# Optimization experiments

Hardware: AMD Instinct MI355X
Metric: run time of the kernel (lower is better)

Reference implementation:

```python
import jax, jax.numpy as jnp
import numpy as np

N, D = 512, 512
MARGIN = 1.0
NUM_CLASSES = 64


def setup_inputs() -> dict:
    key = jax.random.key(0)
    k1, k2 = jax.random.split(key)
    x = jax.random.normal(k1, (N, D), dtype=jnp.float32)
    x = x / jnp.linalg.norm(x, axis=1, keepdims=True)  # l2-normalized embeddings
    target = jax.random.randint(k2, (N,), 0, NUM_CLASSES)
    return {"input": x, "target": target}


def _pairwise_sq_dist(emb):
    # Faithful to pairwise_distance_torch: returns SQUARED distances (no sqrt),
    # clamped at 0, zeroed where <= 0, with zeroed diagonal.
    emb = emb.astype(jnp.float32)
    sq = jnp.sum(emb * emb, axis=1)
    d2 = sq[:, None] + sq[None, :] - 2.0 * (emb @ emb.T)
    d2 = jnp.maximum(d2, 0.0)
    d2 = d2 * (d2 > 0.0).astype(jnp.float32)          # error_mask
    d2 = d2 * (1.0 - jnp.eye(d2.shape[0], dtype=jnp.float32))  # off-diagonal mask
    return d2


def _triplet_semi_hard_loss(embeddings, labels, margin):
    pd = _pairwise_sq_dist(embeddings)                # [N, N]
    n = labels.shape[0]
    adj = labels[:, None] == labels[None, :]          # [N, N]
    adj_not = ~adj

    # mask3[r, i, k] = adj_not[r, k] & (pd[r, k] > pd[r, i])  (anchor r, positive i, candidate k)
    mask3 = adj_not[:, None, :] & (pd[:, None, :] > pd[:, :, None])   # [N, N, N]
    mask3f = mask3.astype(jnp.float32)

    # masked row-wise min over k (semi-hard negative outside the margin band)
    rowmax = jnp.max(pd, axis=1)                      # [N]
    neg_out = jnp.min((pd[:, None, :] - rowmax[:, None, None]) * mask3f, axis=2) + rowmax[:, None]  # [N, N]

    # masked row-wise max over all negatives (fallback when no semi-hard exists)
    rowmin = jnp.min(pd, axis=1, keepdims=True)       # [N, 1]
    neg_in = jnp.max((pd - rowmin) * adj_not.astype(jnp.float32), axis=1, keepdims=True) + rowmin   # [N, 1]

    mask_final = jnp.any(mask3, axis=2)               # [N, N]
    semi_hard = jnp.where(mask_final, neg_out, neg_in)

    mask_pos = adj.astype(jnp.float32) - jnp.eye(n, dtype=jnp.float32)
    num_pos = jnp.sum(mask_pos)
    num_pos = jnp.where(num_pos == 0, num_pos + 1e-5, num_pos)

    loss_mat = margin + pd - semi_hard
    loss = jnp.sum(jnp.maximum(loss_mat * mask_pos, 0.0)) / num_pos
    return loss.astype(embeddings.dtype)


def reference(input, target):
    return _triplet_semi_hard_loss(input, target, MARGIN)
```

## Files before the change

### kernel.cpp

```cpp
#include <hip/hip_runtime.h>
#include <math.h>

namespace {

constexpr int N = 512;
constexpr int D = 512;
constexpr float MARGIN = 1.0f;

__global__ void sq_kernel(const float* __restrict__ x, float* __restrict__ sq,
                          float* __restrict__ acc) {
  const int r = blockIdx.x;
  const int lane = threadIdx.x;
  const float4* xr = reinterpret_cast<const float4*>(x + (size_t)r * D);
  float4 a = xr[lane];
  float4 b = xr[lane + 64];
  float s = a.x * a.x + a.y * a.y + a.z * a.z + a.w * a.w +
            b.x * b.x + b.y * b.y + b.z * b.z + b.w * b.w;
#pragma unroll
  for (int o = 32; o; o >>= 1) s += __shfl_xor(s, o, 64);
  if (lane == 0) sq[r] = s;
  if (r == 0 && lane == 0) {
    acc[0] = 0.0f;
    acc[1] = 0.0f;
  }
}

__global__ void pd_kernel(const float* __restrict__ x, const float* __restrict__ sq,
                          float* __restrict__ pd) {
  __shared__ float As[32][33];
  __shared__ float Bs[32][33];
  const int tx = threadIdx.x & 15;
  const int ty = threadIdx.x >> 4;
  const int bi = blockIdx.y * 32;
  const int bj = blockIdx.x * 32;
  const int lr = threadIdx.x >> 3;
  const int lc = (threadIdx.x & 7) << 2;
  float a00 = 0.f, a01 = 0.f, a10 = 0.f, a11 = 0.f;
  for (int k0 = 0; k0 < D; k0 += 32) {
    float4 va = *reinterpret_cast<const float4*>(&x[(size_t)(bi + lr) * D + k0 + lc]);
    float4 vb = *reinterpret_cast<const float4*>(&x[(size_t)(bj + lr) * D + k0 + lc]);
    As[lr][lc] = va.x; As[lr][lc + 1] = va.y; As[lr][lc + 2] = va.z; As[lr][lc + 3] = va.w;
    Bs[lr][lc] = vb.x; Bs[lr][lc + 1] = vb.y; Bs[lr][lc + 2] = vb.z; Bs[lr][lc + 3] = vb.w;
    __syncthreads();
#pragma unroll
    for (int kk = 0; kk < 32; ++kk) {
      float A0 = As[ty * 2 + 0][kk], A1 = As[ty * 2 + 1][kk];
      float B0 = Bs[tx * 2 + 0][kk], B1 = Bs[tx * 2 + 1][kk];
      a00 = fmaf(A0, B0, a00);
      a01 = fmaf(A0, B1, a01);
      a10 = fmaf(A1, B0, a10);
      a11 = fmaf(A1, B1, a11);
    }
    __syncthreads();
  }
  const int i0 = bi + ty * 2, j0 = bj + tx * 2;
  float accv[2][2] = {{a00, a01}, {a10, a11}};
#pragma unroll
  for (int ri = 0; ri < 2; ++ri) {
#pragma unroll
    for (int cj = 0; cj < 2; ++cj) {
      const int i = i0 + ri, j = j0 + cj;
      float v = sq[i] + sq[j] - 2.0f * accv[ri][cj];
      v = fmaxf(v, 0.0f);
      if (i == j) v = 0.0f;
      pd[(size_t)i * N + j] = v;
    }
  }
}

__global__ void row_kernel(const float* __restrict__ pd, const int* __restrict__ labels,
                           float* __restrict__ acc) {
  const int r = blockIdx.x;
  __shared__ float row[N];
  __shared__ int lab[N];
  __shared__ short pos[N];
  __shared__ int poscount;
  __shared__ float s_red[4];
  __shared__ float s_negin;
  __shared__ float s_loss[4];
  if (threadIdx.x == 0) poscount = 0;
  __syncthreads();
  const int lr = labels[r];
  float mx = 0.0f;
  for (int k = threadIdx.x; k < N; k += 256) {
    float v = pd[(size_t)r * N + k];
    int lk = labels[k];
    row[k] = v;
    lab[k] = lk;
    if (lk != lr) {
      mx = fmaxf(mx, v);
    } else if (k != r) {
      int idx = atomicAdd(&poscount, 1);
      pos[idx] = (short)k;
    }
  }
#pragma unroll
  for (int o = 32; o; o >>= 1) mx = fmaxf(mx, __shfl_xor(mx, o, 64));
  const int wid = threadIdx.x >> 6;
  const int lane = threadIdx.x & 63;
  if (lane == 0) s_red[wid] = mx;
  __syncthreads();
  if (threadIdx.x == 0) {
    s_negin = fmaxf(fmaxf(s_red[0], s_red[1]), fmaxf(s_red[2], s_red[3]));
  }
  __syncthreads();
  const float negin = s_negin;
  const int npos = poscount;
  float wsum = 0.0f;
  for (int p = wid; p < npos; p += 4) {
    const int i = pos[p];
    const float di = row[i];
    float mn = 3.4e38f;
#pragma unroll
    for (int kb = 0; kb < N; kb += 64) {
      const int k = kb + lane;
      const float v = row[k];
      if (lab[k] != lr && v > di) mn = fminf(mn, v);
    }
#pragma unroll
    for (int o = 32; o; o >>= 1) mn = fminf(mn, __shfl_xor(mn, o, 64));
    const float semi = (mn < 1.0e30f) ? mn : negin;
    const float term = fmaxf(MARGIN + di - semi, 0.0f);
    if (lane == 0) wsum += term;
  }
  if (lane == 0) s_loss[wid] = wsum;
  __syncthreads();
  if (threadIdx.x == 0) {
    const float t = s_loss[0] + s_loss[1] + s_loss[2] + s_loss[3];
    atomicAdd(&acc[0], t);
    atomicAdd(&acc[1], (float)npos);
  }
}

__global__ void finalize_kernel(const float* __restrict__ acc, float* __restrict__ out) {
  float np = acc[1];
  if (np == 0.0f) np = 1e-5f;
  out[0] = acc[0] / np;
}

}

extern "C" void kernel_launch(void* const* d_in, const int* in_sizes, int n_in,
                              void* d_out, int out_size, void* d_ws, size_t ws_size,
                              hipStream_t stream) {
  const float* x = (const float*)d_in[0];
  const int* labels = (const int*)d_in[1];
  float* out = (float*)d_out;

  float* pd = (float*)d_ws;
  float* sq = pd + (size_t)N * N;
  float* acc = sq + N;

  sq_kernel<<<N, 64, 0, stream>>>(x, sq, acc);
  pd_kernel<<<dim3(N / 32, N / 32), 256, 0, stream>>>(x, sq, pd);
  row_kernel<<<N, 256, 0, stream>>>(pd, labels, acc);
  finalize_kernel<<<1, 1, 0, stream>>>(acc, out);
}
```

Before: 42.14 us.

## Fuse norm computation into distance GEMM and finalize into row kernel

Drops the separate squared-norm kernel by accumulating row norms inside the distance GEMM tile loads, and drops the finalize kernel by having the last row block, found through an atomic counter, compute the final division. This cuts the launch count from four to two. It also transposes the shared-memory tiles so the inner loop can use float2 reads, vectorizes the pd stores, and uses float2/int2 loads in the row kernel. The cost is a redundant norm computation in every tile and a grid-completion atomic with a threadfence. The accumulators are reset inside the GEMM kernel, which relies on stream ordering.

```diff
diff --git a/kernel.cpp b/kernel.cpp
--- a/kernel.cpp
+++ b/kernel.cpp
@@ -7,69 +7,77 @@
 constexpr int D = 512;
 constexpr float MARGIN = 1.0f;
 
-__global__ void sq_kernel(const float* __restrict__ x, float* __restrict__ sq,
-                          float* __restrict__ acc) {
-  const int r = blockIdx.x;
-  const int lane = threadIdx.x;
-  const float4* xr = reinterpret_cast<const float4*>(x + (size_t)r * D);
-  float4 a = xr[lane];
-  float4 b = xr[lane + 64];
-  float s = a.x * a.x + a.y * a.y + a.z * a.z + a.w * a.w +
-            b.x * b.x + b.y * b.y + b.z * b.z + b.w * b.w;
-#pragma unroll
-  for (int o = 32; o; o >>= 1) s += __shfl_xor(s, o, 64);
-  if (lane == 0) sq[r] = s;
-  if (r == 0 && lane == 0) {
-    acc[0] = 0.0f;
-    acc[1] = 0.0f;
-  }
-}
-
-__global__ void pd_kernel(const float* __restrict__ x, const float* __restrict__ sq,
-                          float* __restrict__ pd) {
-  __shared__ float As[32][33];
-  __shared__ float Bs[32][33];
+__global__ __launch_bounds__(256) void pd_kernel(const float* __restrict__ x,
+                                                 float* __restrict__ pd,
+                                                 float* __restrict__ acc) {
+  __shared__ float As[32][34];
+  __shared__ float Bs[32][34];
+  __shared__ float sA[32];
+  __shared__ float sB[32];
   const int tx = threadIdx.x & 15;
   const int ty = threadIdx.x >> 4;
   const int bi = blockIdx.y * 32;
   const int bj = blockIdx.x * 32;
   const int lr = threadIdx.x >> 3;
   const int lc = (threadIdx.x & 7) << 2;
+
+  if (blockIdx.x == 0 && blockIdx.y == 0 && threadIdx.x < 3) {
+    acc[threadIdx.x] = 0.0f;
+  }
+
+  float ssa = 0.0f, ssb = 0.0f;
   float a00 = 0.f, a01 = 0.f, a10 = 0.f, a11 = 0.f;
   for (int k0 = 0; k0 < D; k0 += 32) {
     float4 va = *reinterpret_cast<const float4*>(&x[(size_t)(bi + lr) * D + k0 + lc]);
     float4 vb = *reinterpret_cast<const float4*>(&x[(size_t)(bj + lr) * D + k0 + lc]);
-    As[lr][lc] = va.x; As[lr][lc + 1] = va.y; As[lr][lc + 2] = va.z; As[lr][lc + 3] = va.w;
-    Bs[lr][lc] = vb.x; Bs[lr][lc + 1] = vb.y; Bs[lr][lc + 2] = vb.z; Bs[lr][lc + 3] = vb.w;
+    ssa += va.x * va.x + va.y * va.y + va.z * va.z + va.w * va.w;
+    ssb += vb.x * vb.x + vb.y * vb.y + vb.z * vb.z + vb.w * vb.w;
+    As[lc + 0][lr] = va.x; As[lc + 1][lr] = va.y; As[lc + 2][lr] = va.z; As[lc + 3][lr] = va.w;
+    Bs[lc + 0][lr] = vb.x; Bs[lc + 1][lr] = vb.y; Bs[lc + 2][lr] = vb.z; Bs[lc + 3][lr] = vb.w;
     __syncthreads();
 #pragma unroll
     for (int kk = 0; kk < 32; ++kk) {
-      float A0 = As[ty * 2 + 0][kk], A1 = As[ty * 2 + 1][kk];
-      float B0 = Bs[tx * 2 + 0][kk], B1 = Bs[tx * 2 + 1][kk];
-      a00 = fmaf(A0, B0, a00);
-      a01 = fmaf(A0, B1, a01);
-      a10 = fmaf(A1, B0, a10);
-      a11 = fmaf(A1, B1, a11);
+      float2 A = *reinterpret_cast<const float2*>(&As[kk][ty * 2]);
+      float2 B = *reinterpret_cast<const float2*>(&Bs[kk][tx * 2]);
+      a00 = fmaf(A.x, B.x, a00);
+      a01 = fmaf(A.x, B.y, a01);
+      a10 = fmaf(A.y, B.x, a10);
+      a11 = fmaf(A.y, B.y, a11);
     }
     __syncthreads();
   }
+#pragma unroll
+  for (int o = 1; o < 8; o <<= 1) {
+    ssa += __shfl_xor(ssa, o, 64);
+    ssb += __shfl_xor(ssb, o, 64);
+  }
+  if ((threadIdx.x & 7) == 0) {
+    sA[lr] = ssa;
+    sB[lr] = ssb;
+  }
+  __syncthreads();
+
   const int i0 = bi + ty * 2, j0 = bj + tx * 2;
   float accv[2][2] = {{a00, a01}, {a10, a11}};
 #pragma unroll
   for (int ri = 0; ri < 2; ++ri) {
-#pragma unroll
-    for (int cj = 0; cj < 2; ++cj) {
-      const int i = i0 + ri, j = j0 + cj;
-      float v = sq[i] + sq[j] - 2.0f * accv[ri][cj];
-      v = fmaxf(v, 0.0f);
-      if (i == j) v = 0.0f;
-      pd[(size_t)i * N + j] = v;
-    }
+    const int i = i0 + ri;
+    float2 o2;
+    float v0 = sA[ty * 2 + ri] + sB[tx * 2 + 0] - 2.0f * accv[ri][0];
+    float v1 = sA[ty * 2 + ri] + sB[tx * 2 + 1] - 2.0f * accv[ri][1];
+    v0 = fmaxf(v0, 0.0f);
+    v1 = fmaxf(v1, 0.0f);
+    if (i == j0 + 0) v0 = 0.0f;
+    if (i == j0 + 1) v1 = 0.0f;
+    o2.x = v0; o2.y = v1;
+    *reinterpret_cast<float2*>(&pd[(size_t)i * N + j0]) = o2;
   }
 }
 
-__global__ void row_kernel(const float* __restrict__ pd, const int* __restrict__ labels,
-                           float* __restrict__ acc) {
+__global__ __launch_bounds__(256) void row_kernel(const float* __restrict__ pd,
+                                                  const int* __restrict__ labels,
+                                                  float* __restrict__ acc,
+                                                  float* __restrict__ out) {
   const int r = blockIdx.x;
   __shared__ float row[N];
   __shared__ int lab[N];
@@ -82,17 +90,17 @@
   __syncthreads();
   const int lr = labels[r];
   float mx = 0.0f;
-  for (int k = threadIdx.x; k < N; k += 256) {
-    float v = pd[(size_t)r * N + k];
-    int lk = labels[k];
-    row[k] = v;
-    lab[k] = lk;
-    if (lk != lr) {
-      mx = fmaxf(mx, v);
-    } else if (k != r) {
-      int idx = atomicAdd(&poscount, 1);
-      pos[idx] = (short)k;
-    }
+  {
+    const int k2 = threadIdx.x;
+    float2 v2 = reinterpret_cast<const float2*>(pd + (size_t)r * N)[k2];
+    int2 l2 = reinterpret_cast<const int2*>(labels)[k2];
+    const int ka = 2 * k2, kb = 2 * k2 + 1;
+    row[ka] = v2.x; row[kb] = v2.y;
+    lab[ka] = l2.x; lab[kb] = l2.y;
+    if (l2.x != lr) mx = fmaxf(mx, v2.x);
+    else if (ka != r) pos[atomicAdd(&poscount, 1)] = (short)ka;
+    if (l2.y != lr) mx = fmaxf(mx, v2.y);
+    else if (kb != r) pos[atomicAdd(&poscount, 1)] = (short)kb;
   }
 #pragma unroll
   for (int o = 32; o; o >>= 1) mx = fmaxf(mx, __shfl_xor(mx, o, 64));
@@ -112,8 +120,8 @@
     const float di = row[i];
     float mn = 3.4e38f;
 #pragma unroll
-    for (int kb = 0; kb < N; kb += 64) {
-      const int k = kb + lane;
+    for (int kb2 = 0; kb2 < N; kb2 += 64) {
+      const int k = kb2 + lane;
       const float v = row[k];
       if (lab[k] != lr && v > di) mn = fminf(mn, v);
     }
@@ -129,13 +137,15 @@
     const float t = s_loss[0] + s_loss[1] + s_loss[2] + s_loss[3];
     atomicAdd(&acc[0], t);
     atomicAdd(&acc[1], (float)npos);
+    __threadfence();
+    unsigned old = atomicAdd(reinterpret_cast<unsigned*>(&acc[2]), 1u);
+    if (old == (unsigned)(gridDim.x - 1)) {
+      float ls = atomicAdd(&acc[0], 0.0f);
+      float np = atomicAdd(&acc[1], 0.0f);
+      if (np == 0.0f) np = 1e-5f;
+      out[0] = ls / np;
+    }
   }
-}
-
-__global__ void finalize_kernel(const float* __restrict__ acc, float* __restrict__ out) {
-  float np = acc[1];
-  if (np == 0.0f) np = 1e-5f;
-  out[0] = acc[0] / np;
 }
 
 }
@@ -148,11 +158,8 @@
   float* out = (float*)d_out;
 
   float* pd = (float*)d_ws;
-  float* sq = pd + (size_t)N * N;
-  float* acc = sq + N;
+  float* acc = pd + (size_t)N * N;
 
-  sq_kernel<<<N, 64, 0, stream>>>(x, sq, acc);
-  pd_kernel<<<dim3(N / 32, N / 32), 256, 0, stream>>>(x, sq, pd);
-  row_kernel<<<N, 256, 0, stream>>>(pd, labels, acc);
-  finalize_kernel<<<1, 1, 0, stream>>>(acc, out);
+  pd_kernel<<<dim3(N / 32, N / 32), 256, 0, stream>>>(x, pd, acc);
+  row_kernel<<<N, 256, 0, stream>>>(pd, labels, acc, out);
 }
```

Measured after the change: 41.41 us. About the same (-1.7%).
